# Kernel optimization log

Hardware: AMD Instinct MI355X
Metric: run time of the kernel (lower is better)

Reference implementation:

```python
import jax, jax.numpy as jnp
import numpy as np

HIDDEN = 4096
N_HEADS = 32
N_KV_HEADS = 8
HEAD_DIM = HIDDEN // N_HEADS
ROPE_BASE = 10000.0


def rotate_half(x):
    x1, x2 = jnp.split(x, 2, axis=-1)
    return jnp.concatenate((-x2, x1), axis=-1)


def rope_cos_sin(seq_len, dtype=jnp.float32):
    inv_freq = 1.0 / (ROPE_BASE ** (jnp.arange(0, HEAD_DIM, 2, dtype=jnp.float32) / HEAD_DIM))
    t = jnp.arange(seq_len, dtype=jnp.float32)
    freqs = jnp.einsum('i,j->ij', t, inv_freq)          # [S, D/2]
    emb = jnp.concatenate((freqs, freqs), axis=-1)       # [S, D]
    return jnp.cos(emb).astype(dtype), jnp.sin(emb).astype(dtype)


def setup_inputs() -> dict:
    key = jax.random.key(0)
    ks = jax.random.split(key, 6)
    bsz, q_len = 2, 2048
    hidden_states = jax.random.normal(ks[0], (bsz, q_len, HIDDEN), dtype=jnp.float32)
    # causal additive mask [bsz, 1, q, kv]
    neg = jnp.finfo(jnp.float32).min
    causal = jnp.where(jnp.tril(jnp.ones((q_len, q_len), dtype=bool)), 0.0, neg)
    attention_mask = jnp.broadcast_to(causal, (bsz, 1, q_len, q_len)).astype(jnp.float32)
    position_ids = jnp.broadcast_to(jnp.arange(q_len, dtype=jnp.int64), (bsz, q_len))
    s = 1.0 / np.sqrt(HIDDEN)
    Wq = jax.random.normal(ks[1], (HIDDEN, N_HEADS * HEAD_DIM), dtype=jnp.float32) * s
    Wk = jax.random.normal(ks[2], (HIDDEN, N_KV_HEADS * HEAD_DIM), dtype=jnp.float32) * s
    Wv = jax.random.normal(ks[3], (HIDDEN, N_KV_HEADS * HEAD_DIM), dtype=jnp.float32) * s
    Wo = jax.random.normal(ks[4], (N_HEADS * HEAD_DIM, HIDDEN), dtype=jnp.float32) * s
    return {"hidden_states": hidden_states, "attention_mask": attention_mask,
            "position_ids": position_ids, "Wq": Wq, "Wk": Wk, "Wv": Wv, "Wo": Wo}


def reference(hidden_states, attention_mask, position_ids, Wq, Wk, Wv, Wo):
    bsz, q_len, _ = hidden_states.shape
    groups = N_HEADS // N_KV_HEADS
    q = (hidden_states @ Wq).reshape(bsz, q_len, N_HEADS, HEAD_DIM).transpose(0, 2, 1, 3)
    k = (hidden_states @ Wk).reshape(bsz, q_len, N_KV_HEADS, HEAD_DIM).transpose(0, 2, 1, 3)
    v = (hidden_states @ Wv).reshape(bsz, q_len, N_KV_HEADS, HEAD_DIM).transpose(0, 2, 1, 3)
    cos, sin = rope_cos_sin(q_len, hidden_states.dtype)
    cos = cos[position_ids][:, None]  # [B,1,S,D]
    sin = sin[position_ids][:, None]
    q = q * cos + rotate_half(q) * sin
    k = k * cos + rotate_half(k) * sin
    # GQA: repeat_interleave KV heads
    k = jnp.repeat(k, groups, axis=1)
    v = jnp.repeat(v, groups, axis=1)
    scores = jnp.einsum('bhqd,bhkd->bhqk', q, k) / np.sqrt(HEAD_DIM)
    scores = scores + attention_mask
    attn = jax.nn.softmax(scores.astype(jnp.float32), axis=-1).astype(q.dtype)
    out = jnp.einsum('bhqk,bhkd->bhqd', attn, v)
    out = out.transpose(0, 2, 1, 3).reshape(bsz, q_len, HIDDEN)
    return out @ Wo
```

## Files before the change

kernel.cpp:

```cpp
#include <hip/hip_runtime.h>
#include <cstdint>
#include <type_traits>

typedef unsigned short u16;
typedef __attribute__((ext_vector_type(8))) short bf16x8;
typedef __attribute__((ext_vector_type(4))) float f32x4;

__device__ __forceinline__ u16 f2bf(float f) {
  unsigned u = __float_as_uint(f);
  u += 0x7fffu + ((u >> 16) & 1u);
  return (u16)(u >> 16);
}
__device__ __forceinline__ float bf2f(u16 h) {
  return __uint_as_float(((unsigned)h) << 16);
}
__device__ __forceinline__ unsigned cvtpk(float lo, float hi) {
  unsigned r;
  asm("v_cvt_pk_bf16_f32 %0, %1, %2" : "=v"(r) : "v"(lo), "v"(hi));
  return r;
}

__device__ __forceinline__ void glds16(const u16* g, u16* l) {
  __builtin_amdgcn_global_load_lds((const __attribute__((address_space(1))) void*)g,
                                   (__attribute__((address_space(3))) void*)l,
                                   16, 0, 0);
}

#define MFMA16(a, b, c) __builtin_amdgcn_mfma_f32_16x16x32_bf16((a), (b), (c), 0, 0, 0)

__global__ __launch_bounds__(256) void k_f32_to_bf16(const float* __restrict__ in,
                                                     u16* __restrict__ out, int n4) {
  int i = blockIdx.x * 256 + threadIdx.x;
  if (i < n4) {
    float4 v = ((const float4*)in)[i];
    ushort4 o;
    o.x = f2bf(v.x); o.y = f2bf(v.y); o.z = f2bf(v.z); o.w = f2bf(v.w);
    ((ushort4*)out)[i] = o;
  }
}

__global__ __launch_bounds__(256) void k_transpose_f32_bf16(const float* __restrict__ in,
                                                            u16* __restrict__ out,
                                                            int R, int C) {
  __shared__ float t[32][33];
  int tx = threadIdx.x & 31, ty = threadIdx.x >> 5;
  int c0 = blockIdx.x * 32, r0 = blockIdx.y * 32;
#pragma unroll
  for (int i = 0; i < 4; ++i)
    t[ty + 8 * i][tx] = in[(size_t)(r0 + ty + 8 * i) * C + c0 + tx];
  __syncthreads();
#pragma unroll
  for (int i = 0; i < 4; ++i)
    out[(size_t)(c0 + ty + 8 * i) * R + r0 + tx] = f2bf(t[tx][ty + 8 * i]);
}

template <typename OutT>
__global__ __launch_bounds__(512, 2) void k_gemm256(const u16* __restrict__ A,
                                                    const u16* __restrict__ B,
                                                    OutT* __restrict__ C,
                                                    int M, int N, int K) {
  __shared__ __align__(16) u16 lds[65536];
  const int tid = threadIdx.x, wave = tid >> 6, lane = tid & 63;
  const int quad = lane >> 4, l15 = lane & 15, l7 = l15 & 7;
  const int wr = wave >> 2, wc = wave & 3;

  const int nwg = gridDim.x * gridDim.y;
  const int bid = blockIdx.y * gridDim.x + blockIdx.x;
  const int swz = (bid & 7) * (nwg >> 3) + (bid >> 3);
  const int m0 = (swz / gridDim.x) * 256, n0 = (swz % gridDim.x) * 256;

  const int lrow = lane >> 3, lx = (lane & 7) ^ lrow;
  const size_t rowK = (size_t)K;
  const u16* Abase = A + (size_t)(m0 + wr * 128 + (wave & 3) * 8 + lrow) * rowK + lx * 8;
  const u16* Bbase = B + (size_t)(n0 + wave * 16 + lrow) * rowK + lx * 8;

  u16* const AT0 = lds;
  u16* const BT0 = lds + 16384;
  u16* const AT1 = lds + 32768;
  u16* const BT1 = lds + 49152;
  const int adst = (wr * 128 + (wave & 3) * 8) * 64;
  const int bdst = wave * 16 * 64;

#define STAGE_A(DST, la, kk) \
  glds16(Abase + (size_t)((la) * 32) * rowK + (kk), (DST) + adst + (la) * 2048)
#define STAGE_B(DST, g, kk)                                                      \
  glds16(Bbase + (size_t)((((g) >> 1) * 128 + ((g) & 1) * 8)) * rowK + (kk),     \
         (DST) + bdst + (((g) >> 1) * 128 + ((g) & 1) * 8) * 64)

  const int aoff = (wr * 128 + l15) * 64;
  const int boff = (wc * 64 + l15) * 64;
  const int ck0 = (quad ^ l7) * 8;
  const int ck1 = ((quad + 4) ^ l7) * 8;

  STAGE_B(BT0, 0, 0); STAGE_B(BT0, 1, 0); STAGE_B(BT0, 2, 0); STAGE_B(BT0, 3, 0);
  STAGE_A(AT0, 0, 0); STAGE_A(AT0, 1, 0); STAGE_A(AT0, 2, 0); STAGE_A(AT0, 3, 0);
  f32x4 acc[8][4] = {};
  asm volatile("s_waitcnt vmcnt(0)" ::: "memory");
  asm volatile("s_barrier" ::: "memory");

  const int nt = K >> 6;
  for (int kt = 0; kt < nt; ++kt) {
    u16* const AT = (kt & 1) ? AT1 : AT0;
    u16* const BT = (kt & 1) ? BT1 : BT0;
    u16* const ATn = (kt & 1) ? AT0 : AT1;
    u16* const BTn = (kt & 1) ? BT0 : BT1;

    if (kt + 1 < nt) {
      const int kk = (kt + 1) << 6;
      STAGE_B(BTn, 0, kk); STAGE_B(BTn, 1, kk);
      STAGE_B(BTn, 2, kk); STAGE_B(BTn, 3, kk);
      STAGE_A(ATn, 0, kk); STAGE_A(ATn, 1, kk);
      STAGE_A(ATn, 2, kk); STAGE_A(ATn, 3, kk);
    }

    bf16x8 bq[4][2];
#pragma unroll
    for (int nf = 0; nf < 4; ++nf) {
      bq[nf][0] = *(const bf16x8*)&BT[boff + nf * 1024 + ck0];
      bq[nf][1] = *(const bf16x8*)&BT[boff + nf * 1024 + ck1];
    }
#pragma unroll
    for (int mp = 0; mp < 4; ++mp) {
      bf16x8 a00 = *(const bf16x8*)&AT[aoff + (2 * mp) * 1024 + ck0];
      bf16x8 a01 = *(const bf16x8*)&AT[aoff + (2 * mp) * 1024 + ck1];
      bf16x8 a10 = *(const bf16x8*)&AT[aoff + (2 * mp + 1) * 1024 + ck0];
      bf16x8 a11 = *(const bf16x8*)&AT[aoff + (2 * mp + 1) * 1024 + ck1];
#pragma unroll
      for (int nf = 0; nf < 4; ++nf) {
        acc[2 * mp][nf] = MFMA16(a00, bq[nf][0], acc[2 * mp][nf]);
        acc[2 * mp][nf] = MFMA16(a01, bq[nf][1], acc[2 * mp][nf]);
        acc[2 * mp + 1][nf] = MFMA16(a10, bq[nf][0], acc[2 * mp + 1][nf]);
        acc[2 * mp + 1][nf] = MFMA16(a11, bq[nf][1], acc[2 * mp + 1][nf]);
      }
    }

    asm volatile("s_waitcnt vmcnt(0)" ::: "memory");
    asm volatile("s_barrier" ::: "memory");
  }
#undef STAGE_A
#undef STAGE_B

#pragma unroll
  for (int mf = 0; mf < 8; ++mf)
#pragma unroll
    for (int nf = 0; nf < 4; ++nf) {
      const int row = m0 + wr * 128 + mf * 16 + quad * 4;
      const int col = n0 + wc * 64 + nf * 16 + l15;
#pragma unroll
      for (int r = 0; r < 4; ++r) {
        float v = acc[mf][nf][r];
        if constexpr (std::is_same<OutT, u16>::value)
          C[(size_t)(row + r) * N + col] = f2bf(v);
        else
          C[(size_t)(row + r) * N + col] = v;
      }
    }
}

__global__ __launch_bounds__(256) void k_rope(u16* __restrict__ qkv) {
  int row = blockIdx.x;
  int s = row & 2047;
  u16* base = qkv + (size_t)row * 6144;
  for (int p = threadIdx.x; p < 2560; p += 256) {
    int d, col;
    if (p < 2048) { d = p & 63; col = (p >> 6) * 128 + d; }
    else { int pk = p - 2048; d = pk & 63; col = 4096 + (pk >> 6) * 128 + d; }
    float f = exp2f((float)d * (-13.287712379549449f / 64.0f));
    float th = (float)s * f;
    float c = cosf(th), sn = sinf(th);
    float x1 = bf2f(base[col]), x2 = bf2f(base[col + 64]);
    base[col]      = f2bf(x1 * c - x2 * sn);
    base[col + 64] = f2bf(x2 * c + x1 * sn);
  }
}

__global__ __launch_bounds__(256) void k_vt(const u16* __restrict__ qkv, u16* __restrict__ vt) {
  __shared__ u16 t[32][33];
  int tx = threadIdx.x & 31, ty = threadIdx.x >> 5;
  int s0 = blockIdx.x * 32, d0 = blockIdx.y * 32, g = blockIdx.z;
  int b = g >> 3, kvh = g & 7;
  const u16* in = qkv + (size_t)(b * 2048) * 6144 + 5120 + kvh * 128;
  u16* out = vt + (size_t)g * 128 * 2048;
#pragma unroll
  for (int i = 0; i < 4; ++i)
    t[ty + 8 * i][tx] = in[(size_t)(s0 + ty + 8 * i) * 6144 + d0 + tx];
  __syncthreads();
#pragma unroll
  for (int i = 0; i < 4; ++i)
    out[(size_t)(d0 + ty + 8 * i) * 2048 + s0 + tx] = t[tx][ty + 8 * i];
}

__global__ __launch_bounds__(256) void k_flash(const u16* __restrict__ qkv,
                                               const u16* __restrict__ vt,
                                               u16* __restrict__ ao) {
  __shared__ __align__(16) u16 Ks[64][128];
  __shared__ __align__(16) u16 Vs[128][64];
  __shared__ __align__(16) u16 Ps[4][16][64];
  const int tid = threadIdx.x, wave = tid >> 6, lane = tid & 63;
  const int quad = lane >> 4, l15 = lane & 15, l7 = l15 & 7;
  const int bh = blockIdx.x, b = bh >> 5, h = bh & 31, kvh = h >> 2;
  const int q0 = (31 - (int)blockIdx.y) * 64;

  bf16x8 aq[4];
  {
    const u16* qp = qkv + (size_t)(b * 2048 + q0 + wave * 16 + l15) * 6144 + h * 128 + quad * 8;
#pragma unroll
    for (int c = 0; c < 4; ++c) aq[c] = *(const bf16x8*)(qp + c * 32);
  }

  f32x4 oacc[8] = {};
  float m_r = -1e30f, l_r = 0.f;

  const u16* kbase = qkv + (size_t)(b * 2048) * 6144 + 4096 + kvh * 128;
  const u16* vbase = vt + (size_t)(b * 8 + kvh) * 128 * 2048;

  const int krow = wave * 4 + (lane >> 4);
  const int kch = (lane & 15) ^ (krow & 7);
  const u16* ksrc0 = kbase + (size_t)krow * 6144 + kch * 8;
  const int vrow = wave * 8 + (lane >> 3);
  const int vch = (lane & 7) ^ (vrow & 7);
  const u16* vsrc0 = vbase + (size_t)vrow * 2048 + vch * 8;
  u16* KsW = &Ks[0][0] + wave * 512;
  u16* VsW = &Vs[0][0] + wave * 512;

  const float SC = 0.12751744f;
  const int qg = q0 + wave * 16 + l15;
  const int nk = q0 / 64 + 1;

  for (int kt = 0; kt < nk; ++kt) {
    const int k0 = kt * 64;
    __syncthreads();
#pragma unroll
    for (int it = 0; it < 4; ++it)
      glds16(ksrc0 + (size_t)(k0 + it * 16) * 6144, KsW + it * 2048);
#pragma unroll
    for (int it = 0; it < 4; ++it)
      glds16(vsrc0 + k0 + it * 65536, VsW + it * 2048);
    __syncthreads();

    f32x4 sacc[4] = {};
    __builtin_amdgcn_s_setprio(1);
#pragma unroll
    for (int c = 0; c < 4; ++c)
#pragma unroll
      for (int nt = 0; nt < 4; ++nt) {
        const bf16x8 bk = *(const bf16x8*)&Ks[nt * 16 + l15][((4 * c + quad) ^ l7) * 8];
        sacc[nt] = __builtin_amdgcn_mfma_f32_16x16x32_bf16(bk, aq[c], sacc[nt], 0, 0, 0);
      }
    __builtin_amdgcn_s_setprio(0);

    float p[16];
    if (kt == nk - 1) {
#pragma unroll
      for (int nt = 0; nt < 4; ++nt)
#pragma unroll
        for (int r = 0; r < 4; ++r) {
          const float v = sacc[nt][r] * SC;
          p[nt * 4 + r] = (k0 + nt * 16 + quad * 4 + r > qg) ? -3e38f : v;
        }
    } else {
#pragma unroll
      for (int nt = 0; nt < 4; ++nt)
#pragma unroll
        for (int r = 0; r < 4; ++r) p[nt * 4 + r] = sacc[nt][r] * SC;
    }

    float rm = p[0];
#pragma unroll
    for (int i = 1; i < 16; ++i) rm = fmaxf(rm, p[i]);
    rm = fmaxf(rm, __shfl_xor(rm, 16, 64));
    rm = fmaxf(rm, __shfl_xor(rm, 32, 64));

    if (__any(rm > m_r + 8.0f)) {
      const float mn = fmaxf(m_r, rm);
      const float alpha = exp2f(m_r - mn);
      m_r = mn;
      l_r *= alpha;
#pragma unroll
      for (int r = 0; r < 4; ++r) {
        const float ar = __shfl(alpha, quad * 4 + r, 64);
#pragma unroll
        for (int o = 0; o < 8; ++o) oacc[o][r] *= ar;
      }
    }

    float rs = 0.f;
#pragma unroll
    for (int i = 0; i < 16; ++i) { p[i] = exp2f(p[i] - m_r); rs += p[i]; }
    rs += __shfl_xor(rs, 16, 64);
    rs += __shfl_xor(rs, 32, 64);
    l_r += rs;

    char* psrow = (char*)&Ps[wave][0][0] + l15 * 128;
#pragma unroll
    for (int nt = 0; nt < 4; ++nt)
#pragma unroll
      for (int pr = 0; pr < 2; ++pr) {
        const unsigned pk = cvtpk(p[nt * 4 + pr * 2], p[nt * 4 + pr * 2 + 1]);
        const int csw = (2 * nt + (quad >> 1)) ^ l7;
        *(unsigned*)(psrow + csw * 16 + (quad & 1) * 8 + pr * 4) = pk;
      }

    __builtin_amdgcn_s_setprio(1);
#pragma unroll
    for (int kc = 0; kc < 2; ++kc) {
      const int cs = (4 * kc + quad) ^ l7;
      const bf16x8 ap = *(const bf16x8*)(psrow + cs * 16);
#pragma unroll
      for (int o = 0; o < 8; ++o) {
        const bf16x8 bv = *(const bf16x8*)&Vs[o * 16 + l15][cs * 8];
        oacc[o] = __builtin_amdgcn_mfma_f32_16x16x32_bf16(ap, bv, oacc[o], 0, 0, 0);
      }
    }
    __builtin_amdgcn_s_setprio(0);
  }

  const float inv = 1.0f / l_r;
  u16* op = ao + (size_t)(b * 2048 + q0 + wave * 16 + quad * 4) * 4096 + h * 128 + l15;
#pragma unroll
  for (int r = 0; r < 4; ++r) {
    const float ir = __shfl(inv, quad * 4 + r, 64);
#pragma unroll
    for (int o = 0; o < 8; ++o)
      op[(size_t)r * 4096 + o * 16] = f2bf(oacc[o][r] * ir);
  }
}

extern "C" void kernel_launch(void* const* d_in, const int* in_sizes, int n_in,
                              void* d_out, int out_size, void* d_ws, size_t ws_size,
                              hipStream_t stream) {
  const float* X  = (const float*)d_in[0];
  const float* Wq = (const float*)d_in[3];
  const float* Wk = (const float*)d_in[4];
  const float* Wv = (const float*)d_in[5];
  const float* Wo = (const float*)d_in[6];
  float* out = (float*)d_out;

  char* ws = (char*)d_ws;
  u16* Xb     = (u16*)(ws);
  u16* WqkvT  = (u16*)(ws + 33554432ull);
  u16* WoT    = (u16*)(ws + 83886080ull);
  u16* QKV    = (u16*)(ws + 117440512ull);
  u16* Vt     = (u16*)(ws + 167772160ull);
  u16* AO     = (u16*)(ws + 176160768ull);

  k_f32_to_bf16<<<16384, 256, 0, stream>>>(X, Xb, 4194304);
  k_transpose_f32_bf16<<<dim3(128, 128), 256, 0, stream>>>(Wq, WqkvT, 4096, 4096);
  k_transpose_f32_bf16<<<dim3(32, 128), 256, 0, stream>>>(Wk, WqkvT + (size_t)4096 * 4096, 4096, 1024);
  k_transpose_f32_bf16<<<dim3(32, 128), 256, 0, stream>>>(Wv, WqkvT + (size_t)5120 * 4096, 4096, 1024);
  k_transpose_f32_bf16<<<dim3(128, 128), 256, 0, stream>>>(Wo, WoT, 4096, 4096);
  k_gemm256<u16><<<dim3(24, 16), 512, 0, stream>>>(Xb, WqkvT, QKV, 4096, 6144, 4096);
  k_rope<<<4096, 256, 0, stream>>>(QKV);
  k_vt<<<dim3(64, 4, 16), 256, 0, stream>>>(QKV, Vt);
  k_flash<<<dim3(64, 32), 256, 0, stream>>>(QKV, Vt, AO);
  k_gemm256<float><<<dim3(16, 16), 512, 0, stream>>>(AO, WoT, out, 4096, 4096, 4096);
}
```

Before: 715.9 us.

## Restructure GEMM main loop into four-phase interleaved load/MFMA pipeline

Replaces the simple double-buffered K loop with a schedule that splits each tile step into four quadrants. Global-to-LDS loads for the next A tile and the B tile two steps ahead are issued between MFMA clusters, with barriers, setprio and partial vmcnt waits. The goal is to hide global load latency and LDS reads behind matrix math instead of stalling on a full vmcnt(0) every iteration. In exchange it adds more barriers per iteration, wraps prefetch indices at the end of K, and relies on careful buffer reuse timing for correctness.

```diff
diff --git a/kernel.cpp b/kernel.cpp
--- a/kernel.cpp
+++ b/kernel.cpp
@@ -71,74 +71,124 @@
 
   const int lrow = lane >> 3, lx = (lane & 7) ^ lrow;
   const size_t rowK = (size_t)K;
-  const u16* Abase = A + (size_t)(m0 + wr * 128 + (wave & 3) * 8 + lrow) * rowK + lx * 8;
-  const u16* Bbase = B + (size_t)(n0 + wave * 16 + lrow) * rowK + lx * 8;
-
-  u16* const AT0 = lds;
-  u16* const BT0 = lds + 16384;
-  u16* const AT1 = lds + 32768;
-  u16* const BT1 = lds + 49152;
-  const int adst = (wr * 128 + (wave & 3) * 8) * 64;
-  const int bdst = wave * 16 * 64;
-
-#define STAGE_A(DST, la, kk) \
-  glds16(Abase + (size_t)((la) * 32) * rowK + (kk), (DST) + adst + (la) * 2048)
-#define STAGE_B(DST, g, kk)                                                      \
-  glds16(Bbase + (size_t)((((g) >> 1) * 128 + ((g) & 1) * 8)) * rowK + (kk),     \
-         (DST) + bdst + (((g) >> 1) * 128 + ((g) & 1) * 8) * 64)
+  const u16* Asrc = A + (size_t)(m0 + wave * 16 + lrow) * rowK + lx * 8;
+  const u16* Bsrc = B + (size_t)(n0 + wave * 16 + lrow) * rowK + lx * 8;
+  const int wv = wave * 1024;
+
+  u16* const AS0 = lds;
+  u16* const AS1 = lds + 16384;
+  u16* const BS0 = lds + 32768;
+  u16* const BS1 = lds + 49152;
+
+#define STG(SRC, SB, h, sub, kk)                                         \
+  glds16((SRC) + (size_t)((h) * 128 + (sub) * 8) * rowK + (kk),          \
+         (SB) + (h) * 8192 + wv + (sub) * 512)
 
   const int aoff = (wr * 128 + l15) * 64;
   const int boff = (wc * 64 + l15) * 64;
   const int ck0 = (quad ^ l7) * 8;
   const int ck1 = ((quad + 4) ^ l7) * 8;
 
-  STAGE_B(BT0, 0, 0); STAGE_B(BT0, 1, 0); STAGE_B(BT0, 2, 0); STAGE_B(BT0, 3, 0);
-  STAGE_A(AT0, 0, 0); STAGE_A(AT0, 1, 0); STAGE_A(AT0, 2, 0); STAGE_A(AT0, 3, 0);
+  STG(Bsrc, BS0, 0, 0, 0); STG(Bsrc, BS0, 0, 1, 0);
+  STG(Bsrc, BS0, 1, 0, 0); STG(Bsrc, BS0, 1, 1, 0);
+  STG(Asrc, AS0, 0, 0, 0); STG(Asrc, AS0, 0, 1, 0);
+  STG(Asrc, AS0, 1, 0, 0); STG(Asrc, AS0, 1, 1, 0);
+  STG(Bsrc, BS1, 0, 0, 64); STG(Bsrc, BS1, 0, 1, 64);
+  STG(Bsrc, BS1, 1, 0, 64); STG(Bsrc, BS1, 1, 1, 64);
   f32x4 acc[8][4] = {};
-  asm volatile("s_waitcnt vmcnt(0)" ::: "memory");
-  asm volatile("s_barrier" ::: "memory");
+  asm volatile("s_waitcnt vmcnt(4)\ns_barrier" ::: "memory");
 
   const int nt = K >> 6;
   for (int kt = 0; kt < nt; ++kt) {
-    u16* const AT = (kt & 1) ? AT1 : AT0;
-    u16* const BT = (kt & 1) ? BT1 : BT0;
-    u16* const ATn = (kt & 1) ? AT0 : AT1;
-    u16* const BTn = (kt & 1) ? BT0 : BT1;
-
-    if (kt + 1 < nt) {
-      const int kk = (kt + 1) << 6;
-      STAGE_B(BTn, 0, kk); STAGE_B(BTn, 1, kk);
-      STAGE_B(BTn, 2, kk); STAGE_B(BTn, 3, kk);
-      STAGE_A(ATn, 0, kk); STAGE_A(ATn, 1, kk);
-      STAGE_A(ATn, 2, kk); STAGE_A(ATn, 3, kk);
-    }
-
-    bf16x8 bq[4][2];
-#pragma unroll
-    for (int nf = 0; nf < 4; ++nf) {
-      bq[nf][0] = *(const bf16x8*)&BT[boff + nf * 1024 + ck0];
-      bq[nf][1] = *(const bf16x8*)&BT[boff + nf * 1024 + ck1];
-    }
-#pragma unroll
-    for (int mp = 0; mp < 4; ++mp) {
-      bf16x8 a00 = *(const bf16x8*)&AT[aoff + (2 * mp) * 1024 + ck0];
-      bf16x8 a01 = *(const bf16x8*)&AT[aoff + (2 * mp) * 1024 + ck1];
-      bf16x8 a10 = *(const bf16x8*)&AT[aoff + (2 * mp + 1) * 1024 + ck0];
-      bf16x8 a11 = *(const bf16x8*)&AT[aoff + (2 * mp + 1) * 1024 + ck1];
-#pragma unroll
-      for (int nf = 0; nf < 4; ++nf) {
-        acc[2 * mp][nf] = MFMA16(a00, bq[nf][0], acc[2 * mp][nf]);
-        acc[2 * mp][nf] = MFMA16(a01, bq[nf][1], acc[2 * mp][nf]);
-        acc[2 * mp + 1][nf] = MFMA16(a10, bq[nf][0], acc[2 * mp + 1][nf]);
-        acc[2 * mp + 1][nf] = MFMA16(a11, bq[nf][1], acc[2 * mp + 1][nf]);
-      }
-    }
-
-    asm volatile("s_waitcnt vmcnt(0)" ::: "memory");
-    asm volatile("s_barrier" ::: "memory");
-  }
-#undef STAGE_A
-#undef STAGE_B
+    u16* const Acur = (kt & 1) ? AS1 : AS0;
+    u16* const Anxt = (kt & 1) ? AS0 : AS1;
+    u16* const Bcur = (kt & 1) ? BS1 : BS0;
+    const int ka = ((kt + 1 < nt) ? (kt + 1) : 0) << 6;
+    const int kb = ((kt + 2 < nt) ? (kt + 2) : (kt + 2 - nt)) << 6;
+
+    bf16x8 aq[4][2], bq[4][2];
+#pragma unroll
+    for (int i = 0; i < 4; ++i) {
+      aq[i][0] = *(const bf16x8*)&Acur[aoff + i * 1024 + ck0];
+      aq[i][1] = *(const bf16x8*)&Acur[aoff + i * 1024 + ck1];
+    }
+#pragma unroll
+    for (int n = 0; n < 2; ++n) {
+      bq[n][0] = *(const bf16x8*)&Bcur[boff + n * 1024 + ck0];
+      bq[n][1] = *(const bf16x8*)&Bcur[boff + n * 1024 + ck1];
+    }
+    STG(Asrc, Anxt, 0, 0, ka); STG(Asrc, Anxt, 0, 1, ka);
+    asm volatile("s_barrier" ::: "memory");
+    asm volatile("s_waitcnt lgkmcnt(0)" ::: "memory");
+    __builtin_amdgcn_sched_barrier(0);
+    __builtin_amdgcn_s_setprio(1);
+#pragma unroll
+    for (int i = 0; i < 4; ++i)
+#pragma unroll
+      for (int n = 0; n < 2; ++n) {
+        acc[i][n] = MFMA16(aq[i][0], bq[n][0], acc[i][n]);
+        acc[i][n] = MFMA16(aq[i][1], bq[n][1], acc[i][n]);
+      }
+    __builtin_amdgcn_s_setprio(0);
+    asm volatile("s_barrier" ::: "memory");
+
+#pragma unroll
+    for (int n = 2; n < 4; ++n) {
+      bq[n][0] = *(const bf16x8*)&Bcur[boff + n * 1024 + ck0];
+      bq[n][1] = *(const bf16x8*)&Bcur[boff + n * 1024 + ck1];
+    }
+    STG(Asrc, Anxt, 1, 0, ka); STG(Asrc, Anxt, 1, 1, ka);
+    asm volatile("s_barrier" ::: "memory");
+    asm volatile("s_waitcnt lgkmcnt(0)" ::: "memory");
+    __builtin_amdgcn_sched_barrier(0);
+    __builtin_amdgcn_s_setprio(1);
+#pragma unroll
+    for (int i = 0; i < 4; ++i)
+#pragma unroll
+      for (int n = 2; n < 4; ++n) {
+        acc[i][n] = MFMA16(aq[i][0], bq[n][0], acc[i][n]);
+        acc[i][n] = MFMA16(aq[i][1], bq[n][1], acc[i][n]);
+      }
+    __builtin_amdgcn_s_setprio(0);
+    asm volatile("s_barrier" ::: "memory");
+
+#pragma unroll
+    for (int i = 0; i < 4; ++i) {
+      aq[i][0] = *(const bf16x8*)&Acur[aoff + (i + 4) * 1024 + ck0];
+      aq[i][1] = *(const bf16x8*)&Acur[aoff + (i + 4) * 1024 + ck1];
+    }
+    STG(Bsrc, Bcur, 0, 0, kb); STG(Bsrc, Bcur, 0, 1, kb);
+    asm volatile("s_barrier" ::: "memory");
+    asm volatile("s_waitcnt lgkmcnt(0)" ::: "memory");
+    __builtin_amdgcn_sched_barrier(0);
+    __builtin_amdgcn_s_setprio(1);
+#pragma unroll
+    for (int i = 0; i < 4; ++i)
+#pragma unroll
+      for (int n = 0; n < 2; ++n) {
+        acc[i + 4][n] = MFMA16(aq[i][0], bq[n][0], acc[i + 4][n]);
+        acc[i + 4][n] = MFMA16(aq[i][1], bq[n][1], acc[i + 4][n]);
+      }
+    __builtin_amdgcn_s_setprio(0);
+    asm volatile("s_barrier" ::: "memory");
+
+    STG(Bsrc, Bcur, 1, 0, kb); STG(Bsrc, Bcur, 1, 1, kb);
+    asm volatile("s_barrier" ::: "memory");
+    __builtin_amdgcn_sched_barrier(0);
+    __builtin_amdgcn_s_setprio(1);
+#pragma unroll
+    for (int i = 0; i < 4; ++i)
+#pragma unroll
+      for (int n = 2; n < 4; ++n) {
+        acc[i + 4][n] = MFMA16(aq[i][0], bq[n][0], acc[i + 4][n]);
+        acc[i + 4][n] = MFMA16(aq[i][1], bq[n][1], acc[i + 4][n]);
+      }
+    __builtin_amdgcn_s_setprio(0);
+    asm volatile("s_waitcnt vmcnt(4)\ns_barrier" ::: "memory");
+  }
+#undef STG
+
+  asm volatile("s_waitcnt vmcnt(0)" ::: "memory");
 
 #pragma unroll
   for (int mf = 0; mf < 8; ++mf)
```

After: 739.2 us. 3.3% more time.

## Load GEMM B fragments directly into registers, halving LDS usage

Applied to the files above, without the earlier changes.

The GEMM kernel no longer stages B tiles through LDS. Each wave loads its B fragments straight from global memory into double-buffered registers one k-tile ahead, and only A stays double-buffered in LDS. This halves shared memory per block and removes the B LDS writes and reads, which may allow more resident blocks. The cost is uncoalesced, redundant global loads of B across the waves that share columns, more register pressure, and a loop unrolled by two that assumes an even tile count.

```diff
diff --git a/kernel.cpp b/kernel.cpp
--- a/kernel.cpp
+++ b/kernel.cpp
@@ -59,7 +59,7 @@
                                                     const u16* __restrict__ B,
                                                     OutT* __restrict__ C,
                                                     int M, int N, int K) {
-  __shared__ __align__(16) u16 lds[65536];
+  __shared__ __align__(16) u16 lds[32768];
   const int tid = threadIdx.x, wave = tid >> 6, lane = tid & 63;
   const int quad = lane >> 4, l15 = lane & 15, l7 = l15 & 7;
   const int wr = wave >> 2, wc = wave & 3;
@@ -72,73 +72,70 @@
   const int lrow = lane >> 3, lx = (lane & 7) ^ lrow;
   const size_t rowK = (size_t)K;
   const u16* Abase = A + (size_t)(m0 + wr * 128 + (wave & 3) * 8 + lrow) * rowK + lx * 8;
-  const u16* Bbase = B + (size_t)(n0 + wave * 16 + lrow) * rowK + lx * 8;
-
-  u16* const AT0 = lds;
-  u16* const BT0 = lds + 16384;
-  u16* const AT1 = lds + 32768;
-  u16* const BT1 = lds + 49152;
+  u16* const AS0 = lds;
+  u16* const AS1 = lds + 16384;
   const int adst = (wr * 128 + (wave & 3) * 8) * 64;
-  const int bdst = wave * 16 * 64;
 
 #define STAGE_A(DST, la, kk) \
   glds16(Abase + (size_t)((la) * 32) * rowK + (kk), (DST) + adst + (la) * 2048)
-#define STAGE_B(DST, g, kk)                                                      \
-  glds16(Bbase + (size_t)((((g) >> 1) * 128 + ((g) & 1) * 8)) * rowK + (kk),     \
-         (DST) + bdst + (((g) >> 1) * 128 + ((g) & 1) * 8) * 64)
+
+  const u16* Bf = B + (size_t)(n0 + wc * 64 + l15) * rowK + quad * 8;
+  const u16* Bp0 = Bf;
+  const u16* Bp1 = Bf + 16 * rowK;
+  const u16* Bp2 = Bf + 32 * rowK;
+  const u16* Bp3 = Bf + 48 * rowK;
 
   const int aoff = (wr * 128 + l15) * 64;
-  const int boff = (wc * 64 + l15) * 64;
   const int ck0 = (quad ^ l7) * 8;
   const int ck1 = ((quad + 4) ^ l7) * 8;
 
-  STAGE_B(BT0, 0, 0); STAGE_B(BT0, 1, 0); STAGE_B(BT0, 2, 0); STAGE_B(BT0, 3, 0);
-  STAGE_A(AT0, 0, 0); STAGE_A(AT0, 1, 0); STAGE_A(AT0, 2, 0); STAGE_A(AT0, 3, 0);
   f32x4 acc[8][4] = {};
+  bf16x8 bqA[4][2], bqB[4][2];
+
+  STAGE_A(AS0, 0, 0); STAGE_A(AS0, 1, 0); STAGE_A(AS0, 2, 0); STAGE_A(AS0, 3, 0);
+  bqA[0][0] = *(const bf16x8*)(Bp0); bqA[0][1] = *(const bf16x8*)(Bp0 + 32);
+  bqA[1][0] = *(const bf16x8*)(Bp1); bqA[1][1] = *(const bf16x8*)(Bp1 + 32);
+  bqA[2][0] = *(const bf16x8*)(Bp2); bqA[2][1] = *(const bf16x8*)(Bp2 + 32);
+  bqA[3][0] = *(const bf16x8*)(Bp3); bqA[3][1] = *(const bf16x8*)(Bp3 + 32);
   asm volatile("s_waitcnt vmcnt(0)" ::: "memory");
   asm volatile("s_barrier" ::: "memory");
 
   const int nt = K >> 6;
-  for (int kt = 0; kt < nt; ++kt) {
-    u16* const AT = (kt & 1) ? AT1 : AT0;
-    u16* const BT = (kt & 1) ? BT1 : BT0;
-    u16* const ATn = (kt & 1) ? AT0 : AT1;
-    u16* const BTn = (kt & 1) ? BT0 : BT1;
-
-    if (kt + 1 < nt) {
-      const int kk = (kt + 1) << 6;
-      STAGE_B(BTn, 0, kk); STAGE_B(BTn, 1, kk);
-      STAGE_B(BTn, 2, kk); STAGE_B(BTn, 3, kk);
-      STAGE_A(ATn, 0, kk); STAGE_A(ATn, 1, kk);
-      STAGE_A(ATn, 2, kk); STAGE_A(ATn, 3, kk);
-    }
-
-    bf16x8 bq[4][2];
-#pragma unroll
-    for (int nf = 0; nf < 4; ++nf) {
-      bq[nf][0] = *(const bf16x8*)&BT[boff + nf * 1024 + ck0];
-      bq[nf][1] = *(const bf16x8*)&BT[boff + nf * 1024 + ck1];
-    }
-#pragma unroll
-    for (int mp = 0; mp < 4; ++mp) {
-      bf16x8 a00 = *(const bf16x8*)&AT[aoff + (2 * mp) * 1024 + ck0];
-      bf16x8 a01 = *(const bf16x8*)&AT[aoff + (2 * mp) * 1024 + ck1];
-      bf16x8 a10 = *(const bf16x8*)&AT[aoff + (2 * mp + 1) * 1024 + ck0];
-      bf16x8 a11 = *(const bf16x8*)&AT[aoff + (2 * mp + 1) * 1024 + ck1];
-#pragma unroll
-      for (int nf = 0; nf < 4; ++nf) {
-        acc[2 * mp][nf] = MFMA16(a00, bq[nf][0], acc[2 * mp][nf]);
-        acc[2 * mp][nf] = MFMA16(a01, bq[nf][1], acc[2 * mp][nf]);
-        acc[2 * mp + 1][nf] = MFMA16(a10, bq[nf][0], acc[2 * mp + 1][nf]);
-        acc[2 * mp + 1][nf] = MFMA16(a11, bq[nf][1], acc[2 * mp + 1][nf]);
-      }
-    }
-
-    asm volatile("s_waitcnt vmcnt(0)" ::: "memory");
-    asm volatile("s_barrier" ::: "memory");
-  }
+
+#define GTILE(KT, ACUR, ANXT, BQC, BQN)                                        \
+  {                                                                            \
+    const int kk = ((KT) + 1 < nt) ? (((KT) + 1) << 6) : 0;                    \
+    STAGE_A(ANXT, 0, kk); STAGE_A(ANXT, 1, kk);                                \
+    STAGE_A(ANXT, 2, kk); STAGE_A(ANXT, 3, kk);                                \
+    BQN[0][0] = *(const bf16x8*)(Bp0 + kk); BQN[0][1] = *(const bf16x8*)(Bp0 + kk + 32); \
+    BQN[1][0] = *(const bf16x8*)(Bp1 + kk); BQN[1][1] = *(const bf16x8*)(Bp1 + kk + 32); \
+    BQN[2][0] = *(const bf16x8*)(Bp2 + kk); BQN[2][1] = *(const bf16x8*)(Bp2 + kk + 32); \
+    BQN[3][0] = *(const bf16x8*)(Bp3 + kk); BQN[3][1] = *(const bf16x8*)(Bp3 + kk + 32); \
+    _Pragma("unroll")                                                          \
+    for (int mp = 0; mp < 4; ++mp) {                                           \
+      bf16x8 a00 = *(const bf16x8*)&ACUR[aoff + (2 * mp) * 1024 + ck0];        \
+      bf16x8 a01 = *(const bf16x8*)&ACUR[aoff + (2 * mp) * 1024 + ck1];        \
+      bf16x8 a10 = *(const bf16x8*)&ACUR[aoff + (2 * mp + 1) * 1024 + ck0];    \
+      bf16x8 a11 = *(const bf16x8*)&ACUR[aoff + (2 * mp + 1) * 1024 + ck1];    \
+      _Pragma("unroll")                                                        \
+      for (int nf = 0; nf < 4; ++nf) {                                         \
+        acc[2 * mp][nf] = MFMA16(a00, BQC[nf][0], acc[2 * mp][nf]);            \
+        acc[2 * mp][nf] = MFMA16(a01, BQC[nf][1], acc[2 * mp][nf]);            \
+        acc[2 * mp + 1][nf] = MFMA16(a10, BQC[nf][0], acc[2 * mp + 1][nf]);    \
+        acc[2 * mp + 1][nf] = MFMA16(a11, BQC[nf][1], acc[2 * mp + 1][nf]);    \
+      }                                                                        \
+    }                                                                          \
+    __builtin_amdgcn_sched_barrier(0);                                         \
+    asm volatile("s_waitcnt vmcnt(0)" ::: "memory");                           \
+    asm volatile("s_barrier" ::: "memory");                                    \
+  }
+
+  for (int kt = 0; kt < nt; kt += 2) {
+    GTILE(kt, AS0, AS1, bqA, bqB)
+    GTILE(kt + 1, AS1, AS0, bqB, bqA)
+  }
+#undef GTILE
 #undef STAGE_A
-#undef STAGE_B
 
 #pragma unroll
   for (int mf = 0; mf < 8; ++mf)
```

Result: slower. 1.010 ms (+41.0%).
